# Kernel tuning notes

Hardware: AMD Instinct MI355X
Metric: run time of the kernel (lower is better)

## Reference

```python
import math
import jax, jax.numpy as jnp
import numpy as np

N_EMBD = 1024
N_HEAD = 16
N_QUERY_SETS = 4
B, T = 8, 1024


def setup_inputs() -> dict:
    key = jax.random.key(0)
    kx, kw1, kw2 = jax.random.split(key, 3)
    C = N_EMBD
    x = jax.random.normal(kx, (B, T, C), dtype=jnp.float32)
    # torch Linear weights are [out_features, in_features]
    W_attn = jax.random.normal(kw1, ((N_QUERY_SETS + 2) * C, C), dtype=jnp.float32) * (1.0 / math.sqrt(C))
    W_proj = jax.random.normal(kw2, (C, N_QUERY_SETS * C), dtype=jnp.float32) * (1.0 / math.sqrt(N_QUERY_SETS * C))
    return {"x": x, "W_attn": W_attn, "W_proj": W_proj}


def reference(x, W_attn, W_proj):
    Bz, Tz, C = x.shape
    hd = C // N_HEAD
    scale = 1.0 / math.sqrt(hd)
    qkv = x @ W_attn.T                       # [B,T,(nqs+2)*C]
    parts = jnp.split(qkv, N_QUERY_SETS + 2, axis=-1)
    k = parts[-2].reshape(Bz, Tz, N_HEAD, hd).transpose(0, 2, 1, 3)  # [B,H,T,hd]
    v = parts[-1].reshape(Bz, Tz, N_HEAD, hd).transpose(0, 2, 1, 3)
    causal = jnp.tril(jnp.ones((Tz, Tz), dtype=bool))
    outs = []
    for g in range(N_QUERY_SETS):  # fixed small structural loop, reuses K/V
        q = parts[g].reshape(Bz, Tz, N_HEAD, hd).transpose(0, 2, 1, 3)
        att = jnp.einsum('bhqd,bhkd->bhqk', q, k) * scale
        att = jnp.where(causal, att, -jnp.inf)
        att = jax.nn.softmax(att, axis=-1)
        y = jnp.einsum('bhqk,bhkd->bhqd', att, v)
        outs.append(y.transpose(0, 2, 1, 3).reshape(Bz, Tz, C))
    combined = jnp.concatenate(outs, axis=-1)  # [B,T,nqs*C]
    return combined @ W_proj.T                 # [B,T,C]
```

## Files before the change

kernel.cpp:

```cpp
#include <hip/hip_runtime.h>


#define DEVI __device__ __forceinline__

typedef __attribute__((ext_vector_type(4)))  float f32x4;
typedef __attribute__((ext_vector_type(16))) float f32x16;
typedef __attribute__((ext_vector_type(8)))  short bf16x8;

static DEVI short f2bf(float f) {
    union { float f; unsigned int i; } c; c.f = f;
    unsigned int i = c.i;
    unsigned int r = i + 0x7FFFu + ((i >> 16) & 1u);
    return (short)(r >> 16);
}

static DEVI unsigned pk2bf(float a, float b) {
    return __builtin_amdgcn_perm(__float_as_uint(b), __float_as_uint(a), 0x07060302u);
}

static DEVI void gload16(const void* g, void* l) {
    __builtin_amdgcn_global_load_lds(
        (const __attribute__((address_space(1))) unsigned int*)g,
        (__attribute__((address_space(3))) unsigned int*)l,
        16, 0, 0);
}

#define BARRIER() do { __builtin_amdgcn_s_barrier(); \
                       __builtin_amdgcn_sched_barrier(0); } while (0)
#define WAITVM(n) do { asm volatile("s_waitcnt vmcnt(%0)" :: "i"(n) : "memory"); \
                       __builtin_amdgcn_sched_barrier(0); } while (0)

__global__ __launch_bounds__(256)
void cvt_bf16(const float* __restrict__ in, short* __restrict__ out, int n8,
              float scale) {
    int i = blockIdx.x * 256 + threadIdx.x;
    if (i >= n8) return;
    const float4* p = (const float4*)in + (size_t)i * 2;
    float4 v0 = p[0], v1 = p[1];
    short r[8] = { f2bf(v0.x * scale), f2bf(v0.y * scale),
                   f2bf(v0.z * scale), f2bf(v0.w * scale),
                   f2bf(v1.x * scale), f2bf(v1.y * scale),
                   f2bf(v1.z * scale), f2bf(v1.w * scale) };
    *(uint4*)(out + (size_t)i * 8) = *(uint4*)r;
}

static DEVI void stage_half(const short* __restrict__ G, int ldg,
                            short* ldsHalf, int tid) {
    #pragma unroll
    for (int i = 0; i < 2; ++i) {
        int c = tid + (i << 9);
        int row = c >> 3;
        int k8 = (c & 7) ^ (((row >> 2) & 1) << 1);
        gload16(G + (size_t)row * ldg + k8 * 8, ldsHalf + ((c >> 6) << 9));
    }
}

static DEVI bf16x8 ldsfrag(const short* half, int lr, int k8r) {
    int off = lr * 64 + ((k8r * 8) ^ (((lr >> 2) & 1) << 4));
    return *(const bf16x8*)(half + off);
}

__global__ __launch_bounds__(512)
void gemm8_bt(const short* __restrict__ A, const short* __restrict__ B,
              short* __restrict__ C, int M, int N, int K, int nwgN) {
    __shared__ short lds[65536];
    short* const ldsA = lds;
    short* const ldsB = lds + 32768;

    const int tid  = threadIdx.x;
    const int lane = tid & 63;
    const int w    = tid >> 6;
    const int wr   = w >> 2;
    const int wc   = w & 3;
    const int l15  = lane & 15;
    const int g4   = lane >> 4;

    const int nwg = gridDim.x;
    const int wg  = blockIdx.x;
    const int swz = (wg & 7) * (nwg >> 3) + (wg >> 3);
    const int tm  = swz / nwgN, tn = swz % nwgN;

    const short* Ag = A + (size_t)tm * 256 * K;
    const short* Bg = B + (size_t)tn * 256 * K;
    const int NT = K >> 6;

    f32x4 acc[8][4] = {};

    stage_half(Ag,                      K, ldsA,               tid);
    stage_half(Ag + (size_t)128 * K,    K, ldsA + 8192,        tid);
    stage_half(Bg,                      K, ldsB,               tid);
    stage_half(Bg + (size_t)128 * K,    K, ldsB + 8192,        tid);
    stage_half(Bg + 64,                 K, ldsB + 16384,       tid);
    stage_half(Bg + (size_t)128 * K + 64, K, ldsB + 16384 + 8192, tid);
    WAITVM(4);
    BARRIER();

    for (int u = 0; u < NT; ++u) {
        const int buf = u & 1;
        const short* Ah = ldsA + buf * 16384 + wr * 8192;
        const short* Bh = ldsB + buf * 16384 + (wc >> 1) * 8192;
        const int lrB = (wc & 1) * 64;
        short* stA = ldsA + (buf ^ 1) * 16384;
        short* stB = ldsB + buf * 16384;
        const short* AgN  = Ag + (size_t)(u + 1) * 64;
        const short* BgN2 = Bg + (size_t)(u + 2) * 64;
        const bool doA = (u + 1 < NT), doB = (u + 2 < NT);

        bf16x8 af[4][2], b0[2][2], b1[2][2];

        #pragma unroll
        for (int f = 0; f < 4; ++f)
            #pragma unroll
            for (int ks = 0; ks < 2; ++ks)
                af[f][ks] = ldsfrag(Ah, f * 16 + l15, ks * 4 + g4);
        #pragma unroll
        for (int fn = 0; fn < 2; ++fn)
            #pragma unroll
            for (int ks = 0; ks < 2; ++ks)
                b0[fn][ks] = ldsfrag(Bh, lrB + fn * 16 + l15, ks * 4 + g4);
        if (doA) stage_half(AgN, K, stA, tid);
        BARRIER();
        __builtin_amdgcn_s_setprio(1);
        #pragma unroll
        for (int f = 0; f < 4; ++f)
            #pragma unroll
            for (int fn = 0; fn < 2; ++fn)
                #pragma unroll
                for (int ks = 0; ks < 2; ++ks)
                    acc[f][fn] = __builtin_amdgcn_mfma_f32_16x16x32_bf16(
                        af[f][ks], b0[fn][ks], acc[f][fn], 0, 0, 0);
        __builtin_amdgcn_s_setprio(0);
        BARRIER();

        #pragma unroll
        for (int fn = 0; fn < 2; ++fn)
            #pragma unroll
            for (int ks = 0; ks < 2; ++ks)
                b1[fn][ks] = ldsfrag(Bh, lrB + 32 + fn * 16 + l15, ks * 4 + g4);
        if (doA) stage_half(AgN + (size_t)128 * K, K, stA + 8192, tid);
        BARRIER();
        __builtin_amdgcn_s_setprio(1);
        #pragma unroll
        for (int f = 0; f < 4; ++f)
            #pragma unroll
            for (int fn = 0; fn < 2; ++fn)
                #pragma unroll
                for (int ks = 0; ks < 2; ++ks)
                    acc[f][2 + fn] = __builtin_amdgcn_mfma_f32_16x16x32_bf16(
                        af[f][ks], b1[fn][ks], acc[f][2 + fn], 0, 0, 0);
        __builtin_amdgcn_s_setprio(0);
        BARRIER();

        #pragma unroll
        for (int f = 0; f < 4; ++f)
            #pragma unroll
            for (int ks = 0; ks < 2; ++ks)
                af[f][ks] = ldsfrag(Ah, 64 + f * 16 + l15, ks * 4 + g4);
        if (doB) stage_half(BgN2, K, stB, tid);
        BARRIER();
        __builtin_amdgcn_s_setprio(1);
        #pragma unroll
        for (int f = 0; f < 4; ++f)
            #pragma unroll
            for (int fn = 0; fn < 2; ++fn)
                #pragma unroll
                for (int ks = 0; ks < 2; ++ks)
                    acc[4 + f][fn] = __builtin_amdgcn_mfma_f32_16x16x32_bf16(
                        af[f][ks], b0[fn][ks], acc[4 + f][fn], 0, 0, 0);
        __builtin_amdgcn_s_setprio(0);
        BARRIER();

        if (doB) stage_half(BgN2 + (size_t)128 * K, K, stB + 8192, tid);
        BARRIER();
        __builtin_amdgcn_s_setprio(1);
        #pragma unroll
        for (int f = 0; f < 4; ++f)
            #pragma unroll
            for (int fn = 0; fn < 2; ++fn)
                #pragma unroll
                for (int ks = 0; ks < 2; ++ks)
                    acc[4 + f][2 + fn] = __builtin_amdgcn_mfma_f32_16x16x32_bf16(
                        af[f][ks], b1[fn][ks], acc[4 + f][2 + fn], 0, 0, 0);
        __builtin_amdgcn_s_setprio(0);
        if (doB) { WAITVM(4); } else { WAITVM(0); }
        BARRIER();
    }

    const size_t r0 = (size_t)tm * 256 + wr * 128 + g4 * 4;
    const int    c0 = tn * 256 + wc * 64 + l15;
    #pragma unroll
    for (int mf = 0; mf < 8; ++mf)
        #pragma unroll
        for (int nf = 0; nf < 4; ++nf)
            #pragma unroll
            for (int j = 0; j < 4; ++j)
                C[(r0 + mf * 16 + j) * N + c0 + nf * 16] = f2bf(acc[mf][nf][j]);
}

template<bool OUT_F32>
__global__ __launch_bounds__(256)
void gemm_bt(const short* __restrict__ A, const short* __restrict__ B,
             void* __restrict__ Cp, int M, int N, int K) {
    __shared__ short As[128 * 32];
    __shared__ short Bs[128 * 32];

    const int tid  = threadIdx.x;
    const int lane = tid & 63;
    const int wid  = tid >> 6;
    const int wr   = wid >> 1;
    const int wc   = wid & 1;
    const int brow = blockIdx.y * 128;
    const int bcol = blockIdx.x * 128;

    const int l15 = lane & 15;
    const int grp = lane >> 4;
    const int sr = lane >> 2;
    const int sc = (lane & 3) ^ ((sr & 1) << 1);

    f32x4 acc[4][4] = {};

    for (int k0 = 0; k0 < K; k0 += 32) {
        #pragma unroll
        for (int it = 0; it < 2; it++) {
            int cb = wid + it * 4;
            int r  = cb * 16 + sr;
            gload16(A + (size_t)(brow + r) * K + k0 + sc * 8, &As[cb * 512]);
            gload16(B + (size_t)(bcol + r) * K + k0 + sc * 8, &Bs[cb * 512]);
        }
        __syncthreads();

        bf16x8 a[4], b[4];
        #pragma unroll
        for (int m = 0; m < 4; m++) {
            int rA = wr * 64 + m * 16 + l15;
            int ch = grp ^ ((rA & 1) << 1);
            a[m] = *(const bf16x8*)(&As[rA * 32 + ch * 8]);
        }
        #pragma unroll
        for (int n = 0; n < 4; n++) {
            int rB = wc * 64 + n * 16 + l15;
            int ch = grp ^ ((rB & 1) << 1);
            b[n] = *(const bf16x8*)(&Bs[rB * 32 + ch * 8]);
        }
        #pragma unroll
        for (int m = 0; m < 4; m++)
            #pragma unroll
            for (int n = 0; n < 4; n++)
                acc[m][n] = __builtin_amdgcn_mfma_f32_16x16x32_bf16(a[m], b[n], acc[m][n], 0, 0, 0);
        __syncthreads();
    }

    const int r0 = brow + wr * 64 + (lane >> 4) * 4;
    const int c0 = bcol + wc * 64 + l15;
    if (OUT_F32) {
        float* C = (float*)Cp;
        #pragma unroll
        for (int m = 0; m < 4; m++)
            #pragma unroll
            for (int n = 0; n < 4; n++)
                #pragma unroll
                for (int j = 0; j < 4; j++)
                    C[(size_t)(r0 + m * 16 + j) * N + c0 + n * 16] = acc[m][n][j];
    } else {
        short* C = (short*)Cp;
        #pragma unroll
        for (int m = 0; m < 4; m++)
            #pragma unroll
            for (int n = 0; n < 4; n++)
                #pragma unroll
                for (int j = 0; j < 4; j++)
                    C[(size_t)(r0 + m * 16 + j) * N + c0 + n * 16] = f2bf(acc[m][n][j]);
    }
}

__global__ __launch_bounds__(512, 4)
void attn_fwd(const short* __restrict__ qkv, short* __restrict__ Y) {
    __shared__ __align__(16) char smem[34816];
    short* const KsB0 = (short*)smem;
    short* const VtB0 = (short*)smem + 4096;
    short* const KsB1 = (short*)smem + 8192;
    short* const VtB1 = (short*)smem + 12288;

    const int tid  = threadIdx.x;
    const int lane = tid & 63;
    const int w    = tid >> 6;
    const int q    = lane & 31;
    const int hf   = lane >> 5;

    const int b  = blockIdx.x >> 4;
    const int h  = blockIdx.x & 15;
    const int qt = (gridDim.y - 1) - blockIdx.y;
    const int g  = w >> 1;
    const int lq = (w & 1) * 32 + q;
    const size_t RS = 6144;
    const int bT = b * 1024;

    bf16x8 qf[4];
    {
        const short* qp = qkv + (size_t)(bT + qt * 64 + lq) * RS + g * 1024 + h * 64 + 8 * hf;
        #pragma unroll
        for (int ks2 = 0; ks2 < 4; ks2++)
            qf[ks2] = *(const bf16x8*)(qp + 16 * ks2);
    }

    f32x16 ot[2] = {};
    float m_run = -3e38f, lsum = 0.f;

    const int kvS   = tid >> 3;
    const int klog  = (tid & 7) ^ (kvS & 7);
    const int d2    = tid >> 4;
    const int ch4   = tid & 15;
    const int vd0   = d2 * 2;
    const int vp0   = (ch4 >> 1) ^ (vd0 & 7);
    const int vp1   = (ch4 >> 1) ^ ((vd0 + 1) & 7);

    const short* const kvtile = qkv + (size_t)bT * RS + h * 64;

    {
        const short* vp = kvtile + (size_t)(ch4 * 4) * RS + 5120 + vd0;
        unsigned v0 = *(const unsigned*)(vp);
        unsigned v1 = *(const unsigned*)(vp + RS);
        unsigned v2 = *(const unsigned*)(vp + 2 * RS);
        unsigned v3 = *(const unsigned*)(vp + 3 * RS);
        gload16(kvtile + (size_t)kvS * RS + 4096 + klog * 8, KsB0 + w * 512);
        uint2 lo, hi2;
        lo.x  = __builtin_amdgcn_perm(v1, v0, 0x05040100u);
        lo.y  = __builtin_amdgcn_perm(v3, v2, 0x05040100u);
        hi2.x = __builtin_amdgcn_perm(v1, v0, 0x07060302u);
        hi2.y = __builtin_amdgcn_perm(v3, v2, 0x07060302u);
        char* vb = (char*)VtB0;
        *(uint2*)(vb + vd0 * 128 + vp0 * 16 + (ch4 & 1) * 8)       = lo;
        *(uint2*)(vb + (vd0 + 1) * 128 + vp1 * 16 + (ch4 & 1) * 8) = hi2;
    }
    __syncthreads();

    for (int kvt = 0; kvt <= qt; kvt++) {
        short* const Ksc = (kvt & 1) ? KsB1 : KsB0;
        short* const Vtc = (kvt & 1) ? VtB1 : VtB0;
        short* const Ksn = (kvt & 1) ? KsB0 : KsB1;
        short* const Vtn = (kvt & 1) ? VtB0 : VtB1;
        const bool pf = (kvt < qt);

        unsigned v0, v1, v2, v3;
        if (pf) {
            const short* vp = kvtile + (size_t)((kvt + 1) * 64 + ch4 * 4) * RS + 5120 + vd0;
            v0 = *(const unsigned*)(vp);
            v1 = *(const unsigned*)(vp + RS);
            v2 = *(const unsigned*)(vp + 2 * RS);
            v3 = *(const unsigned*)(vp + 3 * RS);
            gload16(kvtile + (size_t)((kvt + 1) * 64 + kvS) * RS + 4096 + klog * 8,
                    Ksn + w * 512);
        }

        f32x16 stt[2] = {};
        __builtin_amdgcn_s_setprio(1);
        #pragma unroll
        for (int sti = 0; sti < 2; sti++) {
            const int kvr = sti * 32 + q;
            #pragma unroll
            for (int ks2 = 0; ks2 < 4; ks2++) {
                const int phys = (2 * ks2 + hf) ^ (kvr & 7);
                bf16x8 kf = *(const bf16x8*)(Ksc + kvr * 64 + phys * 8);
                stt[sti] = __builtin_amdgcn_mfma_f32_32x32x16_bf16(kf, qf[ks2], stt[sti], 0, 0, 0);
            }
        }
        __builtin_amdgcn_s_setprio(0);

        if (kvt == qt) {
            #pragma unroll
            for (int sti = 0; sti < 2; sti++)
                #pragma unroll
                for (int r = 0; r < 16; r++) {
                    int kvl = sti * 32 + (r & 3) + 8 * (r >> 2) + 4 * hf;
                    if (kvl > lq) stt[sti][r] = -3e38f;
                }
        }

        float pm[4] = { -3e38f, -3e38f, -3e38f, -3e38f };
        #pragma unroll
        for (int r = 0; r < 16; r++)
            pm[r & 3] = fmaxf(pm[r & 3], fmaxf(stt[0][r], stt[1][r]));
        float mx = fmaxf(fmaxf(pm[0], pm[1]), fmaxf(pm[2], pm[3]));
        mx = fmaxf(mx, __shfl_xor(mx, 32));

        if (!__all(mx - m_run <= 8.0f)) {
            const float mn = fmaxf(m_run, mx);
            const float alpha = __builtin_amdgcn_exp2f(m_run - mn);
            m_run = mn;
            lsum *= alpha;
            ot[0] *= alpha;
            ot[1] *= alpha;
        }

        float sp[4] = { 0.f, 0.f, 0.f, 0.f };
        #pragma unroll
        for (int sti = 0; sti < 2; sti++)
            #pragma unroll
            for (int r = 0; r < 16; r++) {
                float e = __builtin_amdgcn_exp2f(stt[sti][r] - m_run);
                stt[sti][r] = e;
                sp[r & 3] += e;
            }
        float sum = (sp[0] + sp[1]) + (sp[2] + sp[3]);
        sum += __shfl_xor(sum, 32);
        lsum += sum;

        if (pf) {
            uint2 lo, hi2;
            lo.x  = __builtin_amdgcn_perm(v1, v0, 0x05040100u);
            lo.y  = __builtin_amdgcn_perm(v3, v2, 0x05040100u);
            hi2.x = __builtin_amdgcn_perm(v1, v0, 0x07060302u);
            hi2.y = __builtin_amdgcn_perm(v3, v2, 0x07060302u);
            char* vb = (char*)Vtn;
            *(uint2*)(vb + vd0 * 128 + vp0 * 16 + (ch4 & 1) * 8)       = lo;
            *(uint2*)(vb + (vd0 + 1) * 128 + vp1 * 16 + (ch4 & 1) * 8) = hi2;
        }

        bf16x8 pf4[4];
        #pragma unroll
        for (int ks = 0; ks < 4; ks++) {
            const int sti = ks >> 1, base = 8 * (ks & 1);
            unsigned X0 = pk2bf(stt[sti][base + 0], stt[sti][base + 1]);
            unsigned X1 = pk2bf(stt[sti][base + 2], stt[sti][base + 3]);
            unsigned Y0 = pk2bf(stt[sti][base + 4], stt[sti][base + 5]);
            unsigned Y1 = pk2bf(stt[sti][base + 6], stt[sti][base + 7]);
            asm("v_permlane32_swap_b32 %0, %1" : "+v"(X0), "+v"(Y0));
            asm("v_permlane32_swap_b32 %0, %1" : "+v"(X1), "+v"(Y1));
            unsigned t[4] = { X0, X1, Y0, Y1 };
            pf4[ks] = *(bf16x8*)t;
        }

        __builtin_amdgcn_s_setprio(1);
        #pragma unroll
        for (int dsub = 0; dsub < 2; dsub++) {
            const int dr = dsub * 32 + q;
            #pragma unroll
            for (int ks = 0; ks < 4; ks++) {
                const int phys = (2 * ks + hf) ^ (dr & 7);
                bf16x8 vf = *(const bf16x8*)(Vtc + dr * 64 + phys * 8);
                ot[dsub] = __builtin_amdgcn_mfma_f32_32x32x16_bf16(vf, pf4[ks], ot[dsub], 0, 0, 0);
            }
        }
        __builtin_amdgcn_s_setprio(0);

        __syncthreads();
    }

    unsigned* obuf = (unsigned*)smem;
    const float inv = 1.0f / lsum;
    const int SQ = g * 64 + lq;
    #pragma unroll
    for (int dsub = 0; dsub < 2; dsub++)
        #pragma unroll
        for (int r = 0; r < 16; r += 2) {
            int d = dsub * 32 + (r & 3) + 8 * (r >> 2) + 4 * hf;
            unsigned pk = ((unsigned)(unsigned short)f2bf(ot[dsub][r] * inv)) |
                          (((unsigned)(unsigned short)f2bf(ot[dsub][r + 1] * inv)) << 16);
            obuf[SQ * 34 + (d >> 1)] = pk;
        }
    __syncthreads();
    {
        const int SQ2 = tid >> 1, seg = tid & 1;
        const int g2 = SQ2 >> 6, lq2 = SQ2 & 63;
        const size_t row = (size_t)(bT + qt * 64 + lq2);
        const unsigned* src = obuf + SQ2 * 34 + seg * 16;
        unsigned* dst = (unsigned*)(Y + row * 4096 + g2 * 1024 + h * 64 + seg * 32);
        #pragma unroll
        for (int k = 0; k < 4; k++) {
            uint2 u0 = *(const uint2*)(src + 4 * k);
            uint2 u1 = *(const uint2*)(src + 4 * k + 2);
            uint4 t; t.x = u0.x; t.y = u0.y; t.z = u1.x; t.w = u1.y;
            *(uint4*)(dst + 4 * k) = t;
        }
    }
}

extern "C" void kernel_launch(void* const* d_in, const int* in_sizes, int n_in,
                              void* d_out, int out_size, void* d_ws, size_t ws_size,
                              hipStream_t stream) {
    const float* x  = (const float*)d_in[0];
    const float* Wa = (const float*)d_in[1];
    const float* Wp = (const float*)d_in[2];
    float* out = (float*)d_out;

    short* qkv = (short*)d_ws;
    short* Yb  = qkv + (size_t)8192 * 6144;
    short* xb  = Yb;
    short* Wab = Yb + (size_t)8192 * 1024;
    short* Wpb = qkv;

    const float QS = 0.18033688011112042f;
    dim3 blk(256);
    cvt_bf16<<<dim3(8192 * 1024 / 8 / 256), blk, 0, stream>>>(x, xb, 8192 * 1024 / 8, 1.0f);
    cvt_bf16<<<dim3(4096 * 1024 / 8 / 256), blk, 0, stream>>>(Wa, Wab, 4096 * 1024 / 8, QS);
    cvt_bf16<<<dim3(2048 * 1024 / 8 / 256), blk, 0, stream>>>(
        Wa + (size_t)4096 * 1024, Wab + (size_t)4096 * 1024, 2048 * 1024 / 8, 1.0f);
    gemm8_bt<<<dim3(768), dim3(512), 0, stream>>>(xb, Wab, qkv, 8192, 6144, 1024, 24);
    attn_fwd<<<dim3(128, 16), dim3(512), 0, stream>>>(qkv, Yb);
    cvt_bf16<<<dim3(1024 * 4096 / 8 / 256), blk, 0, stream>>>(Wp, Wpb, 1024 * 4096 / 8, 1.0f);
    gemm_bt<true><<<dim3(8, 64), blk, 0, stream>>>(Yb, Wpb, (void*)out, 8192, 1024, 4096);
}
```

Measured before the change: 370.8 us.

## Replace output projection GEMM with pipelined 256x128 8-wave kernel; merge input conversions

Swaps the simple 128x128 single-buffered projection GEMM for an 8-wave kernel with 256x128 tiles, 64-wide K steps, double-buffered global-to-LDS staging, set-priority MFMA phases and a swizzled tile order. The aim is to hide load latency and raise MFMA utilisation on the K=4096 projection. The three fp32-to-bf16 conversion launches for x and W_attn are also fused into one kernel to save launch overhead. The trade-off is only 256 workgroups for the projection, which may leave some CUs idle, plus higher LDS use per block.

```diff
diff --git a/kernel.cpp b/kernel.cpp
--- a/kernel.cpp
+++ b/kernel.cpp
@@ -29,6 +29,29 @@
                        __builtin_amdgcn_sched_barrier(0); } while (0)
 #define WAITVM(n) do { asm volatile("s_waitcnt vmcnt(%0)" :: "i"(n) : "memory"); \
                        __builtin_amdgcn_sched_barrier(0); } while (0)
+
+__global__ __launch_bounds__(256)
+void cvt_all(const float* __restrict__ x, const float* __restrict__ Wa,
+             short* __restrict__ dst, float qs) {
+    const int i = blockIdx.x * 256 + threadIdx.x;
+    const int X8 = 1048576, WQ8 = 524288;
+    const float* src;
+    float scale = 1.0f;
+    if (i < X8) {
+        src = x + (size_t)i * 8;
+    } else {
+        int j = i - X8;
+        src = Wa + (size_t)j * 8;
+        if (j < WQ8) scale = qs;
+    }
+    const float4* p = (const float4*)src;
+    float4 v0 = p[0], v1 = p[1];
+    short r[8] = { f2bf(v0.x * scale), f2bf(v0.y * scale),
+                   f2bf(v0.z * scale), f2bf(v0.w * scale),
+                   f2bf(v1.x * scale), f2bf(v1.y * scale),
+                   f2bf(v1.z * scale), f2bf(v1.w * scale) };
+    *(uint4*)(dst + (size_t)i * 8) = *(uint4*)r;
+}
 
 __global__ __launch_bounds__(256)
 void cvt_bf16(const float* __restrict__ in, short* __restrict__ out, int n8,
@@ -197,80 +220,106 @@
                 C[(r0 + mf * 16 + j) * N + c0 + nf * 16] = f2bf(acc[mf][nf][j]);
 }
 
-template<bool OUT_F32>
-__global__ __launch_bounds__(256)
-void gemm_bt(const short* __restrict__ A, const short* __restrict__ B,
-             void* __restrict__ Cp, int M, int N, int K) {
-    __shared__ short As[128 * 32];
-    __shared__ short Bs[128 * 32];
+__global__ __launch_bounds__(512)
+void gemm8_bt2(const short* __restrict__ A, const short* __restrict__ B,
+               float* __restrict__ C, int M, int N, int K) {
+    __shared__ short lds[49152];
+    short* const ldsA = lds;
+    short* const ldsB = lds + 32768;
 
     const int tid  = threadIdx.x;
     const int lane = tid & 63;
-    const int wid  = tid >> 6;
-    const int wr   = wid >> 1;
-    const int wc   = wid & 1;
-    const int brow = blockIdx.y * 128;
-    const int bcol = blockIdx.x * 128;
-
-    const int l15 = lane & 15;
-    const int grp = lane >> 4;
-    const int sr = lane >> 2;
-    const int sc = (lane & 3) ^ ((sr & 1) << 1);
-
-    f32x4 acc[4][4] = {};
-
-    for (int k0 = 0; k0 < K; k0 += 32) {
-        #pragma unroll
-        for (int it = 0; it < 2; it++) {
-            int cb = wid + it * 4;
-            int r  = cb * 16 + sr;
-            gload16(A + (size_t)(brow + r) * K + k0 + sc * 8, &As[cb * 512]);
-            gload16(B + (size_t)(bcol + r) * K + k0 + sc * 8, &Bs[cb * 512]);
-        }
-        __syncthreads();
-
-        bf16x8 a[4], b[4];
-        #pragma unroll
-        for (int m = 0; m < 4; m++) {
-            int rA = wr * 64 + m * 16 + l15;
-            int ch = grp ^ ((rA & 1) << 1);
-            a[m] = *(const bf16x8*)(&As[rA * 32 + ch * 8]);
-        }
-        #pragma unroll
-        for (int n = 0; n < 4; n++) {
-            int rB = wc * 64 + n * 16 + l15;
-            int ch = grp ^ ((rB & 1) << 1);
-            b[n] = *(const bf16x8*)(&Bs[rB * 32 + ch * 8]);
-        }
-        #pragma unroll
-        for (int m = 0; m < 4; m++)
-            #pragma unroll
-            for (int n = 0; n < 4; n++)
-                acc[m][n] = __builtin_amdgcn_mfma_f32_16x16x32_bf16(a[m], b[n], acc[m][n], 0, 0, 0);
-        __syncthreads();
-    }
-
-    const int r0 = brow + wr * 64 + (lane >> 4) * 4;
-    const int c0 = bcol + wc * 64 + l15;
-    if (OUT_F32) {
-        float* C = (float*)Cp;
-        #pragma unroll
-        for (int m = 0; m < 4; m++)
-            #pragma unroll
-            for (int n = 0; n < 4; n++)
-                #pragma unroll
-                for (int j = 0; j < 4; j++)
-                    C[(size_t)(r0 + m * 16 + j) * N + c0 + n * 16] = acc[m][n][j];
-    } else {
-        short* C = (short*)Cp;
-        #pragma unroll
-        for (int m = 0; m < 4; m++)
-            #pragma unroll
-            for (int n = 0; n < 4; n++)
-                #pragma unroll
-                for (int j = 0; j < 4; j++)
-                    C[(size_t)(r0 + m * 16 + j) * N + c0 + n * 16] = f2bf(acc[m][n][j]);
-    }
+    const int w    = tid >> 6;
+    const int wr   = w >> 2;
+    const int wc   = w & 3;
+    const int l15  = lane & 15;
+    const int g4   = lane >> 4;
+
+    const int nwg = gridDim.x;
+    const int wg  = blockIdx.x;
+    const int swz = (wg & 7) * (nwg >> 3) + (wg >> 3);
+    const int tm  = swz >> 3, tn = swz & 7;
+
+    const short* Ag = A + (size_t)tm * 256 * K;
+    const short* Bg = B + (size_t)tn * 128 * K;
+    const int NT = K >> 6;
+
+    f32x4 acc[8][2] = {};
+
+    stage_half(Ag,                   K, ldsA,        tid);
+    stage_half(Ag + (size_t)128 * K, K, ldsA + 8192, tid);
+    stage_half(Bg,                   K, ldsB,        tid);
+    stage_half(Bg + 64,              K, ldsB + 8192, tid);
+    WAITVM(2);
+    BARRIER();
+
+    for (int u = 0; u < NT; ++u) {
+        const int buf = u & 1;
+        const short* Ah = ldsA + buf * 16384 + wr * 8192;
+        const short* Bb = ldsB + buf * 8192;
+        short* stA = ldsA + (buf ^ 1) * 16384;
+        short* stB = ldsB + buf * 8192;
+        const short* AgN  = Ag + (size_t)(u + 1) * 64;
+        const short* BgN2 = Bg + (size_t)(u + 2) * 64;
+        const bool doA = (u + 1 < NT), doB = (u + 2 < NT);
+
+        bf16x8 af[4][2], b[2][2];
+
+        #pragma unroll
+        for (int f = 0; f < 4; ++f)
+            #pragma unroll
+            for (int ks = 0; ks < 2; ++ks)
+                af[f][ks] = ldsfrag(Ah, f * 16 + l15, ks * 4 + g4);
+        #pragma unroll
+        for (int fn = 0; fn < 2; ++fn)
+            #pragma unroll
+            for (int ks = 0; ks < 2; ++ks)
+                b[fn][ks] = ldsfrag(Bb, wc * 32 + fn * 16 + l15, ks * 4 + g4);
+        if (doA) stage_half(AgN, K, stA, tid);
+        BARRIER();
+        __builtin_amdgcn_s_setprio(1);
+        #pragma unroll
+        for (int f = 0; f < 4; ++f)
+            #pragma unroll
+            for (int fn = 0; fn < 2; ++fn)
+                #pragma unroll
+                for (int ks = 0; ks < 2; ++ks)
+                    acc[f][fn] = __builtin_amdgcn_mfma_f32_16x16x32_bf16(
+                        af[f][ks], b[fn][ks], acc[f][fn], 0, 0, 0);
+        __builtin_amdgcn_s_setprio(0);
+        BARRIER();
+
+        #pragma unroll
+        for (int f = 0; f < 4; ++f)
+            #pragma unroll
+            for (int ks = 0; ks < 2; ++ks)
+                af[f][ks] = ldsfrag(Ah, 64 + f * 16 + l15, ks * 4 + g4);
+        if (doA) stage_half(AgN + (size_t)128 * K, K, stA + 8192, tid);
+        if (doB) stage_half(BgN2, K, stB, tid);
+        BARRIER();
+        __builtin_amdgcn_s_setprio(1);
+        #pragma unroll
+        for (int f = 0; f < 4; ++f)
+            #pragma unroll
+            for (int fn = 0; fn < 2; ++fn)
+                #pragma unroll
+                for (int ks = 0; ks < 2; ++ks)
+                    acc[4 + f][fn] = __builtin_amdgcn_mfma_f32_16x16x32_bf16(
+                        af[f][ks], b[fn][ks], acc[4 + f][fn], 0, 0, 0);
+        __builtin_amdgcn_s_setprio(0);
+        if (doB) { WAITVM(2); } else { WAITVM(0); }
+        BARRIER();
+    }
+
+    const size_t r0 = (size_t)tm * 256 + wr * 128 + g4 * 4;
+    const int    c0 = tn * 128 + wc * 32 + l15;
+    #pragma unroll
+    for (int mf = 0; mf < 8; ++mf)
+        #pragma unroll
+        for (int nf = 0; nf < 2; ++nf)
+            #pragma unroll
+            for (int j = 0; j < 4; ++j)
+                C[(r0 + mf * 16 + j) * N + c0 + nf * 16] = acc[mf][nf][j];
 }
 
 __global__ __launch_bounds__(512, 4)
@@ -491,12 +540,9 @@
 
     const float QS = 0.18033688011112042f;
     dim3 blk(256);
-    cvt_bf16<<<dim3(8192 * 1024 / 8 / 256), blk, 0, stream>>>(x, xb, 8192 * 1024 / 8, 1.0f);
-    cvt_bf16<<<dim3(4096 * 1024 / 8 / 256), blk, 0, stream>>>(Wa, Wab, 4096 * 1024 / 8, QS);
-    cvt_bf16<<<dim3(2048 * 1024 / 8 / 256), blk, 0, stream>>>(
-        Wa + (size_t)4096 * 1024, Wab + (size_t)4096 * 1024, 2048 * 1024 / 8, 1.0f);
+    cvt_all<<<dim3((8192 + 6144) * 1024 / 8 / 256), blk, 0, stream>>>(x, Wa, xb, QS);
     gemm8_bt<<<dim3(768), dim3(512), 0, stream>>>(xb, Wab, qkv, 8192, 6144, 1024, 24);
     attn_fwd<<<dim3(128, 16), dim3(512), 0, stream>>>(qkv, Yb);
     cvt_bf16<<<dim3(1024 * 4096 / 8 / 256), blk, 0, stream>>>(Wp, Wpb, 1024 * 4096 / 8, 1.0f);
-    gemm_bt<true><<<dim3(8, 64), blk, 0, stream>>>(Yb, Wpb, (void*)out, 8192, 1024, 4096);
-}
+    gemm8_bt2<<<dim3(256), dim3(512), 0, stream>>>(Yb, Wpb, out, 8192, 1024, 4096);
+}
```

After: 339.2 us. -8.5%, faster.
